# Kernel tuning notes

Measured on AMD Instinct MI355X. Metric: run time of the kernel, lower is better.

Reference implementation:

```python
import jax, jax.numpy as jnp
import numpy as np

MARGIN = 0.3  # from init_kwargs
N, D = 4096, 128


def _pairwise_sqdist(a, b):
    # ||a_i - b_j||^2 via the matmul identity; avoids an [N, N, D] intermediate.
    a2 = jnp.sum(a * a, axis=1)[:, None]
    b2 = jnp.sum(b * b, axis=1)[None, :]
    return a2 + b2 - 2.0 * (a @ b.T)


def setup_inputs() -> dict:
    key = jax.random.key(0)
    k1, k2 = jax.random.split(key)
    pair1 = jax.random.normal(k1, (N, D), dtype=jnp.float32)
    pair2 = jax.random.normal(k2, (N, D), dtype=jnp.float32)
    return {"pair1": pair1, "pair2": pair2}


def reference(pair1, pair2):
    n = pair1.shape[0]
    # positive distance per anchor: ||pair1[i] - pair2[i]||^2
    dist_ap = jnp.sum((pair1 - pair2) ** 2, axis=1)  # [N]
    D1 = _pairwise_sqdist(pair1, pair1)  # dist_an1[i, j]
    D2 = _pairwise_sqdist(pair1, pair2)  # dist_an2[i, j]
    L1 = jax.nn.relu(dist_ap[:, None] - D1 + MARGIN)  # [N, N]
    L2 = jax.nn.relu(dist_ap[:, None] - D2 + MARGIN)  # [N, N]
    # exclude j == i (the original `continue`); relu outputs are >= 0 and the
    # original hard-mining max starts at 0.0, so zeroing the diagonal is exact.
    offdiag = 1.0 - jnp.eye(n, dtype=L1.dtype)
    L1m = L1 * offdiag
    L2m = L2 * offdiag
    # online hard example mining: max loss per anchor over all 2*(N-1) negatives
    sub_loss = jnp.mean(jnp.maximum(jnp.max(L1m, axis=1), jnp.max(L2m, axis=1)))
    # average over all counted triplets: cnt = 2 * N * (N - 1)
    all_loss = (jnp.sum(L1m) + jnp.sum(L2m)) / (2.0 * n * (n - 1))
    return (sub_loss, all_loss)
```

## Files before the change

kernel.cpp:

```cpp
#include <hip/hip_runtime.h>
#include <hip/hip_bf16.h>

#define NN 4096
#define DD 128
#define MARGIN_F 0.3f
#define JC 256
#define RB 256
#define GX (NN / JC)
#define GY (NN / RB)
#define NT (JC / 16)

typedef __attribute__((ext_vector_type(8))) short bf16x8;
typedef __attribute__((ext_vector_type(4))) float f32x4;
typedef __attribute__((ext_vector_type(2))) float f32x2;


__device__ __forceinline__ ushort f2bf(float f) {
  __hip_bfloat16 h = __float2bfloat16(f);
  return *reinterpret_cast<ushort*>(&h);
}

__device__ __forceinline__ void gload_lds16(const ushort* g, ushort* l) {
  __builtin_amdgcn_global_load_lds(
      (const __attribute__((address_space(1))) void*)g,
      (__attribute__((address_space(3))) void*)l, 16, 0, 0);
}

__global__ __launch_bounds__(256) void ptl_prep(
    const float* __restrict__ p1, const float* __restrict__ p2,
    ushort* __restrict__ p1t, ushort* __restrict__ p2t,
    float* __restrict__ a2, float* __restrict__ b2, float* __restrict__ c,
    unsigned int* __restrict__ rowmax, float* __restrict__ sumpart) {
  int row = blockIdx.x * 4 + (threadIdx.x >> 6);
  int lane = threadIdx.x & 63;
  float2 x = ((const float2*)(p1 + (size_t)row * DD))[lane];
  float2 y = ((const float2*)(p2 + (size_t)row * DD))[lane];
  ushort2 xb, yb;
  xb.x = f2bf(x.x); xb.y = f2bf(x.y);
  yb.x = f2bf(y.x); yb.y = f2bf(y.y);
  int k = lane * 2;
  size_t idx = (size_t)(row >> 4) * 2048 + (size_t)(k >> 5) * 512 +
               (size_t)((k & 31) >> 3) * 128 + (size_t)(row & 15) * 8 +
               (size_t)(k & 7);
  *(ushort2*)(p1t + idx) = xb;
  *(ushort2*)(p2t + idx) = yb;

  float sa = x.x * x.x + x.y * x.y;
  float sb = y.x * y.x + y.y * y.y;
  float d0 = x.x - y.x, d1 = x.y - y.y;
  float sd = d0 * d0 + d1 * d1;
#pragma unroll
  for (int off = 32; off > 0; off >>= 1) {
    sa += __shfl_down(sa, off);
    sb += __shfl_down(sb, off);
    sd += __shfl_down(sd, off);
  }
  if (lane == 0) {
    a2[row] = sa;
    b2[row] = sb;
    c[row] = sd - sa + MARGIN_F;
    rowmax[row] = 0u;
  }
  if (blockIdx.x == 0 && threadIdx.x < 16) sumpart[threadIdx.x] = 0.f;
}

__global__ __launch_bounds__(512) void ptl_mfma(
    const ushort* __restrict__ p1t, const ushort* __restrict__ p2t,
    const float* __restrict__ a2v, const float* __restrict__ b2v,
    const float* __restrict__ cvv, unsigned int* __restrict__ rowmax,
    float* __restrict__ sumpart) {
  const int tid = threadIdx.x;
  const int w = tid >> 6;
  const int lane = tid & 63;
  const int col16 = lane & 15;
  const int quad = lane >> 4;
  const int rowBase = blockIdx.y * RB + w * 32;
  const int jBase = blockIdx.x * JC;
  const int lofs = quad * 128 + col16 * 8;

  __shared__ __align__(16) ushort ldsB[2][NT][2048];
  __shared__ float wsum[8];

  {
    const int p0 = w * 2;
#pragma unroll
    for (int arr = 0; arr < 2; ++arr) {
      const ushort* gsrc = (arr ? p2t : p1t) +
                           (size_t)((jBase >> 4) + p0) * 2048 + lane * 8;
#pragma unroll
      for (int pp = 0; pp < 2; ++pp)
#pragma unroll
        for (int ch = 0; ch < 4; ++ch)
          gload_lds16(gsrc + pp * 2048 + ch * 512,
                      &ldsB[arr][p0 + pp][ch * 512 + lane * 8]);
    }
  }

  bf16x8 afr[2][4];
#pragma unroll
  for (int st = 0; st < 2; ++st) {
    const ushort* pa = p1t + ((size_t)(rowBase >> 4) + st) * 2048 + lofs;
#pragma unroll
    for (int s = 0; s < 4; ++s) afr[st][s] = *(const bf16x8*)(pa + s * 512);
  }

  float cv[2][4];
#pragma unroll
  for (int st = 0; st < 2; ++st)
#pragma unroll
    for (int r = 0; r < 4; ++r) cv[st][r] = cvv[rowBase + st * 16 + quad * 4 + r];

  f32x2 lsum2 = {0.f, 0.f};
  f32x2 rmax2[2][4];
#pragma unroll
  for (int st = 0; st < 2; ++st)
#pragma unroll
    for (int r = 0; r < 4; ++r) rmax2[st][r] = (f32x2){0.f, 0.f};

  __syncthreads();

#pragma unroll
  for (int jt = 0; jt < NT; ++jt) {
    bf16x8 b1[4], b2[4];
#pragma unroll
    for (int s = 0; s < 4; ++s) {
      b1[s] = *(const bf16x8*)&ldsB[0][jt][s * 512 + lofs];
      b2[s] = *(const bf16x8*)&ldsB[1][jt][s * 512 + lofs];
    }
    f32x4 acc[2][2];
#pragma unroll
    for (int st = 0; st < 2; ++st)
#pragma unroll
      for (int m = 0; m < 2; ++m) acc[st][m] = (f32x4){0.f, 0.f, 0.f, 0.f};
#pragma unroll
    for (int s = 0; s < 4; ++s) {
      acc[0][0] = __builtin_amdgcn_mfma_f32_16x16x32_bf16(afr[0][s], b1[s], acc[0][0], 0, 0, 0);
      acc[1][0] = __builtin_amdgcn_mfma_f32_16x16x32_bf16(afr[1][s], b1[s], acc[1][0], 0, 0, 0);
      acc[0][1] = __builtin_amdgcn_mfma_f32_16x16x32_bf16(afr[0][s], b2[s], acc[0][1], 0, 0, 0);
      acc[1][1] = __builtin_amdgcn_mfma_f32_16x16x32_bf16(afr[1][s], b2[s], acc[1][1], 0, 0, 0);
    }

    const int jcol = jBase + jt * 16 + col16;
    f32x2 nj = { a2v[jcol], b2v[jcol] };
#pragma unroll
    for (int st = 0; st < 2; ++st) {
      const bool diagT = (jBase + jt * 16) == (rowBase + st * 16);
#pragma unroll
      for (int r = 0; r < 4; ++r) {
        f32x2 t = { acc[st][0][r], acc[st][1][r] };
        f32x2 v = t * 2.f + (cv[st][r] - nj);
        v.x = fmaxf(v.x, 0.f);
        v.y = fmaxf(v.y, 0.f);
        if (diagT && col16 == quad * 4 + r) v = (f32x2){0.f, 0.f};
        lsum2 += v;
        rmax2[st][r].x = fmaxf(rmax2[st][r].x, v.x);
        rmax2[st][r].y = fmaxf(rmax2[st][r].y, v.y);
      }
    }
  }

  float lsum = lsum2.x + lsum2.y;
  float rmax[2][4];
#pragma unroll
  for (int st = 0; st < 2; ++st)
#pragma unroll
    for (int r = 0; r < 4; ++r)
      rmax[st][r] = fmaxf(rmax2[st][r].x, rmax2[st][r].y);

#pragma unroll
  for (int off = 8; off > 0; off >>= 1)
#pragma unroll
    for (int st = 0; st < 2; ++st)
#pragma unroll
      for (int r = 0; r < 4; ++r)
        rmax[st][r] = fmaxf(rmax[st][r], __shfl_xor(rmax[st][r], off));
  if (col16 == 0) {
#pragma unroll
    for (int st = 0; st < 2; ++st)
#pragma unroll
      for (int r = 0; r < 4; ++r)
        atomicMax(&rowmax[rowBase + st * 16 + quad * 4 + r],
                  __float_as_uint(rmax[st][r]));
  }

#pragma unroll
  for (int off = 32; off > 0; off >>= 1) lsum += __shfl_down(lsum, off);
  if (lane == 0) wsum[w] = lsum;
  __syncthreads();
  if (tid == 0) {
    float s = 0.f;
#pragma unroll
    for (int i = 0; i < 8; ++i) s += wsum[i];
    const int bid = blockIdx.y * GX + blockIdx.x;
    atomicAdd(&sumpart[bid & 15], s);
  }
}

__global__ __launch_bounds__(256) void ptl_fin(
    const unsigned int* __restrict__ rowmax, const float* __restrict__ sumpart,
    float* __restrict__ out) {
  float sm = 0.f;
#pragma unroll
  for (int it = 0; it < 4; ++it) {
    uint4 u = ((const uint4*)rowmax)[it * 256 + threadIdx.x];
    sm += __uint_as_float(u.x) + __uint_as_float(u.y) +
          __uint_as_float(u.z) + __uint_as_float(u.w);
  }
#pragma unroll
  for (int off = 32; off > 0; off >>= 1) sm += __shfl_down(sm, off);
  __shared__ float wm[4];
  if ((threadIdx.x & 63) == 0) wm[threadIdx.x >> 6] = sm;
  __syncthreads();
  if (threadIdx.x == 0) {
    float sp = 0.f;
#pragma unroll
    for (int i = 0; i < 16; ++i) sp += sumpart[i];
    out[0] = (wm[0] + wm[1] + wm[2] + wm[3]) / (float)NN;
    out[1] = sp / (2.0f * (float)NN * (float)(NN - 1));
  }
}

extern "C" void kernel_launch(void* const* d_in, const int* in_sizes, int n_in,
                              void* d_out, int out_size, void* d_ws, size_t ws_size,
                              hipStream_t stream) {
  const float* p1 = (const float*)d_in[0];
  const float* p2 = (const float*)d_in[1];
  ushort* p1t = (ushort*)d_ws;
  ushort* p2t = p1t + (size_t)NN * DD;
  float* a2 = (float*)(p2t + (size_t)NN * DD);
  float* b2 = a2 + NN;
  float* c = b2 + NN;
  unsigned int* rowmax = (unsigned int*)(c + NN);
  float* sumpart = (float*)(rowmax + NN);

  ptl_prep<<<NN / 4, 256, 0, stream>>>(p1, p2, p1t, p2t, a2, b2, c,
                                       rowmax, sumpart);

  dim3 grid(GX, GY);
  ptl_mfma<<<grid, 512, 0, stream>>>(p1t, p2t, a2, b2, c, rowmax, sumpart);

  ptl_fin<<<1, 256, 0, stream>>>(rowmax, sumpart, (float*)d_out);
}
```

Before: 93.30 us.

## Double-buffer B tiles in LDS with per-tile async prefetch and narrower column blocks

Previously each block loaded its whole 256-column B chunk (128KB of LDS) before any compute. Now the column chunk per block is halved, and LDS holds two 16-column tiles. The next tile is fetched with global_load_lds while the current one is consumed, so the upfront load stall is hidden and LDS use drops, allowing more blocks to be resident. The cost is a block-wide barrier on every tile iteration, and twice as many blocks doing A-fragment loads and rowmax atomics.

```diff
diff --git a/kernel.cpp b/kernel.cpp
--- a/kernel.cpp
+++ b/kernel.cpp
@@ -4,7 +4,7 @@
 #define NN 4096
 #define DD 128
 #define MARGIN_F 0.3f
-#define JC 256
+#define JC 128
 #define RB 256
 #define GX (NN / JC)
 #define GY (NN / RB)
@@ -78,23 +78,17 @@
   const int jBase = blockIdx.x * JC;
   const int lofs = quad * 128 + col16 * 8;
 
-  __shared__ __align__(16) ushort ldsB[2][NT][2048];
+  __shared__ __align__(16) ushort ldsB[2][2][2048];
   __shared__ float wsum[8];
 
-  {
-    const int p0 = w * 2;
-#pragma unroll
-    for (int arr = 0; arr < 2; ++arr) {
-      const ushort* gsrc = (arr ? p2t : p1t) +
-                           (size_t)((jBase >> 4) + p0) * 2048 + lane * 8;
-#pragma unroll
-      for (int pp = 0; pp < 2; ++pp)
-#pragma unroll
-        for (int ch = 0; ch < 4; ++ch)
-          gload_lds16(gsrc + pp * 2048 + ch * 512,
-                      &ldsB[arr][p0 + pp][ch * 512 + lane * 8]);
-    }
-  }
+  const int arr = w >> 2;
+  const int qtr = w & 3;
+  const ushort* gB = (arr ? p2t : p1t) + (size_t)(jBase >> 4) * 2048 +
+                     qtr * 512 + lane * 8;
+  ushort* lB0 = &ldsB[0][arr][qtr * 512 + lane * 8];
+  ushort* lB1 = &ldsB[1][arr][qtr * 512 + lane * 8];
+
+  gload_lds16(gB, lB0);
 
   bf16x8 afr[2][4];
 #pragma unroll
@@ -117,15 +111,18 @@
 #pragma unroll
     for (int r = 0; r < 4; ++r) rmax2[st][r] = (f32x2){0.f, 0.f};
 
-  __syncthreads();
-
 #pragma unroll
   for (int jt = 0; jt < NT; ++jt) {
+    const int cur = jt & 1;
+    __syncthreads();
+    if (jt + 1 < NT)
+      gload_lds16(gB + (size_t)(jt + 1) * 2048, cur ? lB0 : lB1);
+
     bf16x8 b1[4], b2[4];
 #pragma unroll
     for (int s = 0; s < 4; ++s) {
-      b1[s] = *(const bf16x8*)&ldsB[0][jt][s * 512 + lofs];
-      b2[s] = *(const bf16x8*)&ldsB[1][jt][s * 512 + lofs];
+      b1[s] = *(const bf16x8*)&ldsB[cur][0][s * 512 + lofs];
+      b2[s] = *(const bf16x8*)&ldsB[cur][1][s * 512 + lofs];
     }
     f32x4 acc[2][2];
 #pragma unroll
```

Result: faster. 80.33 us (-13.9%).
